# Kernel optimization log

Hardware: AMD Instinct MI355X
Metric: run time of the kernel (lower is better)

Reference implementation:

```python
import jax, jax.numpy as jnp
import numpy as np
from jax import lax

T, B, H = 1024, 128, 512   # num_tokens, batch, encoder hidden
A, K, F = 128, 32, 31      # attention hidden, conv filters, filter length


def setup_inputs() -> dict:
    key = jax.random.key(0)
    ks = jax.random.split(key, 8)
    s = 0.05  # param init scale for numerical stability of tanh
    encoded_tokens = jax.random.normal(ks[0], (T, B, H), jnp.float32)
    query = jax.random.normal(ks[1], (B, H), jnp.float32)
    prev = jax.random.uniform(ks[2], (T, B), jnp.float32)
    previous_alignment = prev / jnp.sum(prev, axis=0, keepdims=True)  # prob-like alignment
    conv_filter = jax.random.normal(ks[3], (K, 1, F), jnp.float32) * s
    W_loc = jax.random.normal(ks[4], (K, A), jnp.float32) * s
    W_q = jax.random.normal(ks[5], (H, A), jnp.float32) * s
    W_k = jax.random.normal(ks[6], (H, A), jnp.float32) * s
    v = jax.random.normal(ks[7], (A,), jnp.float32) * s
    return {"encoded_tokens": encoded_tokens, "query": query,
            "previous_alignment": previous_alignment, "conv_filter": conv_filter,
            "W_loc": W_loc, "W_q": W_q, "W_k": W_k, "v": v}


def reference(encoded_tokens, query, previous_alignment, conv_filter, W_loc, W_q, W_k, v):
    pad = (conv_filter.shape[-1] - 1) // 2
    # Location features: conv1d over token axis of previous alignment.
    # previous_alignment [T,B] -> [B,1,T]; conv_filter [K,1,F] -> loc [B,K,T]
    loc = lax.conv_general_dilated(previous_alignment.T[:, None, :], conv_filter,
                                   window_strides=(1,), padding=[(pad, pad)],
                                   dimension_numbers=("NCH", "OIH", "NCH"))
    proc_loc = jnp.einsum("bkt,ka->tba", loc, W_loc)              # [T,B,A]
    proc_query = query @ W_q                                       # [B,A]
    proc_keys = jnp.einsum("tbh,ha->tba", encoded_tokens, W_k)    # [T,B,A]
    # Additive (Bahdanau) score with tanh nonlinearity.
    score = jnp.einsum("tba,a->tb", jnp.tanh(proc_keys + proc_loc + proc_query[None]), v)
    alignment = jax.nn.softmax(score, axis=0)                      # softmax over tokens [T,B]
    context = jnp.einsum("tb,tbh->bh", alignment, encoded_tokens)  # [B,H]
    return context, alignment
```

## Files before the change

### kernel.cpp

```cpp
#include <hip/hip_runtime.h>
#include <hip/hip_bf16.h>
#include <math.h>

#define T_DIM 1024
#define B_DIM 128
#define H_DIM 512
#define A_DIM 128
#define K_DIM 32
#define F_DIM 31

#define WS_PQ    0
#define WS_SCORE 16384
#define WS_WKHI  147456
#define WS_WKLO  180224
#define WS_WCT   212992
#define WS_PART  147456

typedef __attribute__((ext_vector_type(8)))  short bf16x8;
typedef __attribute__((ext_vector_type(16))) float f32x16;

__device__ __forceinline__ ushort f2bf(float x) {
  unsigned u = __float_as_uint(x);
  u += 0x7FFFu + ((u >> 16) & 1u);
  return (ushort)(u >> 16);
}
__device__ __forceinline__ float bf2f(ushort h) {
  return __uint_as_float(((unsigned)h) << 16);
}
__device__ __forceinline__ float fast_tanh(float x) {
  float xc = fminf(10.f, fmaxf(-10.f, x));
  float e2 = __expf(2.f * xc);
  return __fdividef(e2 - 1.f, e2 + 1.f);
}

__global__ __launch_bounds__(256) void prep_kernel(
    const float* __restrict__ query, const float* __restrict__ conv_filter,
    const float* __restrict__ W_loc, const float* __restrict__ W_q,
    const float* __restrict__ W_k, float* __restrict__ ws)
{
  int blk = blockIdx.x, tid = threadIdx.x;
  if (blk < 128) {
    __shared__ float red[256];
    int a = tid & 127, half = tid >> 7;
    const float* q = query + blk * H_DIM + half * 256;
    const float* w = W_q + (size_t)(half * 256) * A_DIM + a;
    float s = 0.f;
    #pragma unroll 8
    for (int h = 0; h < 256; ++h) s = fmaf(q[h], w[(size_t)h * A_DIM], s);
    red[tid] = s;
    __syncthreads();
    if (tid < 128) ws[WS_PQ + blk * A_DIM + tid] = red[tid] + red[tid + 128];
  } else if (blk == 128) {
    ushort* wct = (ushort*)(ws + WS_WCT);
    for (int it = 0; it < 16; ++it) {
      int e = tid + it * 256;
      int f = e >> 7, a = e & 127;
      float s = 0.f;
      if (f < F_DIM) {
        #pragma unroll
        for (int k = 0; k < K_DIM; ++k)
          s += conv_filter[k * F_DIM + f] * W_loc[k * A_DIM + a];
      }
      wct[a * 32 + f] = f2bf(s);
    }
  } else {
    ushort* wkhi = (ushort*)(ws + WS_WKHI);
    ushort* wklo = (ushort*)(ws + WS_WKLO);
    int h0 = (blk - 129) * 16;
    int a = tid & 127, hh = tid >> 7;
    #pragma unroll
    for (int j = 0; j < 8; ++j) {
      int h = h0 + hh * 8 + j;
      float x = W_k[(size_t)h * A_DIM + a];
      ushort hi = f2bf(x);
      float lo = x - bf2f(hi);
      wkhi[a * H_DIM + h] = hi;
      wklo[a * H_DIM + h] = f2bf(lo);
    }
  }
}

__global__ __launch_bounds__(256, 2) void score_kernel(
    const float* __restrict__ enc, const float* __restrict__ ws_f,
    const float* __restrict__ prev, const float* __restrict__ vvec,
    float* __restrict__ score)
{
  __shared__ ushort smA_hi[256 * 32];
  __shared__ ushort smA_lo[256 * 32];
  __shared__ ushort smB_hi[128 * 32];
  __shared__ ushort smB_lo[128 * 32];
  __shared__ float  prevL[32 * 128];

  const ushort* wkhi = (const ushort*)(ws_f + WS_WKHI);
  const ushort* wklo = (const ushort*)(ws_f + WS_WKLO);
  const ushort* wct  = (const ushort*)(ws_f + WS_WCT);
  const float*  pq   = ws_f + WS_PQ;

  const int tid = threadIdx.x;
  const int t0 = blockIdx.x * 2;
  const int R0 = blockIdx.x * 256;
  const int lane = tid & 63, wv = tid >> 6;
  const int l31 = lane & 31, g = lane >> 5;
  const int wrow = wv * 64;

  f32x16 acc[2][4];
  #pragma unroll
  for (int mf = 0; mf < 2; ++mf)
    #pragma unroll
    for (int nf = 0; nf < 4; ++nf)
      acc[mf][nf] = (f32x16)(0.f);

  #pragma unroll
  for (int it = 0; it < 4; ++it) {
    int seg = tid + it * 256;
    int rr = seg >> 5, c4 = (seg & 31) << 2;
    int t = t0 - 15 + rr;
    float4 val = make_float4(0.f, 0.f, 0.f, 0.f);
    if (t >= 0 && t < T_DIM) val = *(const float4*)(prev + t * B_DIM + c4);
    *(float4*)(prevL + rr * 128 + c4) = val;
  }

  for (int hc = 0; hc < H_DIM; hc += 32) {
    __syncthreads();
    #pragma unroll
    for (int it = 0; it < 8; ++it) {
      int row = it * 32 + (tid >> 3);
      int sub = tid & 7;
      float4 v = *(const float4*)(enc + (size_t)(R0 + row) * H_DIM + hc + sub * 4);
      ushort4 hi4, lo4;
      hi4.x = f2bf(v.x); lo4.x = f2bf(v.x - bf2f(hi4.x));
      hi4.y = f2bf(v.y); lo4.y = f2bf(v.y - bf2f(hi4.y));
      hi4.z = f2bf(v.z); lo4.z = f2bf(v.z - bf2f(hi4.z));
      hi4.w = f2bf(v.w); lo4.w = f2bf(v.w - bf2f(hi4.w));
      int chunk = sub >> 1;
      int boff = row * 64 + ((chunk ^ ((row >> 1) & 3)) << 4) + ((sub & 1) << 3);
      *(ushort4*)((char*)smA_hi + boff) = hi4;
      *(ushort4*)((char*)smA_lo + boff) = lo4;
    }
    #pragma unroll
    for (int it = 0; it < 2; ++it) {
      int a = it * 64 + (tid >> 2);
      int q = tid & 3;
      uint4 vh = *(const uint4*)(wkhi + (size_t)a * H_DIM + hc + q * 8);
      uint4 vl = *(const uint4*)(wklo + (size_t)a * H_DIM + hc + q * 8);
      int boff = a * 64 + ((q ^ ((a >> 1) & 3)) << 4);
      *(uint4*)((char*)smB_hi + boff) = vh;
      *(uint4*)((char*)smB_lo + boff) = vl;
    }
    __syncthreads();
    #pragma unroll
    for (int kk = 0; kk < 2; ++kk) {
      bf16x8 ah[2], al[2];
      #pragma unroll
      for (int mf = 0; mf < 2; ++mf) {
        int row = wrow + mf * 32 + l31;
        int boff = row * 64 + (((kk * 2 + g) ^ ((row >> 1) & 3)) << 4);
        ah[mf] = *(const bf16x8*)((const char*)smA_hi + boff);
        al[mf] = *(const bf16x8*)((const char*)smA_lo + boff);
      }
      #pragma unroll
      for (int nf = 0; nf < 4; ++nf) {
        int a = nf * 32 + l31;
        int boff = a * 64 + (((kk * 2 + g) ^ ((a >> 1) & 3)) << 4);
        bf16x8 bh = *(const bf16x8*)((const char*)smB_hi + boff);
        bf16x8 bl = *(const bf16x8*)((const char*)smB_lo + boff);
        #pragma unroll
        for (int mf = 0; mf < 2; ++mf) {
          acc[mf][nf] = __builtin_amdgcn_mfma_f32_32x32x16_bf16(ah[mf], bh, acc[mf][nf], 0, 0, 0);
          acc[mf][nf] = __builtin_amdgcn_mfma_f32_32x32x16_bf16(ah[mf], bl, acc[mf][nf], 0, 0, 0);
          acc[mf][nf] = __builtin_amdgcn_mfma_f32_32x32x16_bf16(al[mf], bh, acc[mf][nf], 0, 0, 0);
        }
      }
    }
  }

  __syncthreads();
  {
    int trow = tid >> 7, bcol = tid & 127;
    #pragma unroll
    for (int q = 0; q < 4; ++q) {
      bf16x8 pk;
      #pragma unroll
      for (int e = 0; e < 8; ++e) {
        int f = q * 8 + e;
        float pv = (f < F_DIM) ? prevL[(trow + f) * 128 + bcol] : 0.f;
        pk[e] = (short)f2bf(pv);
      }
      int boff = tid * 64 + ((q ^ ((tid >> 1) & 3)) << 4);
      *(bf16x8*)((char*)smA_hi + boff) = pk;
    }
    #pragma unroll
    for (int it = 0; it < 2; ++it) {
      int a = it * 64 + (tid >> 2);
      int q = tid & 3;
      uint4 vv = *(const uint4*)(wct + a * 32 + q * 8);
      *(uint4*)((char*)smB_hi + a * 64 + ((q ^ ((a >> 1) & 3)) << 4)) = vv;
    }
  }
  __syncthreads();
  #pragma unroll
  for (int kk = 0; kk < 2; ++kk) {
    bf16x8 ah[2];
    #pragma unroll
    for (int mf = 0; mf < 2; ++mf) {
      int row = wrow + mf * 32 + l31;
      int boff = row * 64 + (((kk * 2 + g) ^ ((row >> 1) & 3)) << 4);
      ah[mf] = *(const bf16x8*)((const char*)smA_hi + boff);
    }
    #pragma unroll
    for (int nf = 0; nf < 4; ++nf) {
      int a = nf * 32 + l31;
      int boff = a * 64 + (((kk * 2 + g) ^ ((a >> 1) & 3)) << 4);
      bf16x8 bh = *(const bf16x8*)((const char*)smB_hi + boff);
      #pragma unroll
      for (int mf = 0; mf < 2; ++mf)
        acc[mf][nf] = __builtin_amdgcn_mfma_f32_32x32x16_bf16(ah[mf], bh, acc[mf][nf], 0, 0, 0);
    }
  }

  float vval[4];
  #pragma unroll
  for (int nf = 0; nf < 4; ++nf) vval[nf] = vvec[nf * 32 + l31];
  #pragma unroll
  for (int mf = 0; mf < 2; ++mf) {
    #pragma unroll
    for (int reg = 0; reg < 16; ++reg) {
      int row = wrow + mf * 32 + (reg & 3) + 8 * (reg >> 2) + 4 * g;
      int b = row & 127;
      float s = 0.f;
      #pragma unroll
      for (int nf = 0; nf < 4; ++nf) {
        float u = acc[mf][nf][reg] + pq[b * A_DIM + nf * 32 + l31];
        s = fmaf(fast_tanh(u), vval[nf], s);
      }
      s += __shfl_xor(s, 1); s += __shfl_xor(s, 2); s += __shfl_xor(s, 4);
      s += __shfl_xor(s, 8); s += __shfl_xor(s, 16);
      if (l31 == 0) {
        int t = t0 + (row >> 7);
        score[b * T_DIM + t] = s;
      }
    }
  }
}

__global__ __launch_bounds__(256) void softmax_kernel(
    float* __restrict__ score, float* __restrict__ out_align)
{
  __shared__ float red[8];
  int b = blockIdx.x, tid = threadIdx.x;
  float v0[4];
  #pragma unroll
  for (int i = 0; i < 4; ++i) v0[i] = score[b * T_DIM + tid + i * 256];
  float m = fmaxf(fmaxf(v0[0], v0[1]), fmaxf(v0[2], v0[3]));
  #pragma unroll
  for (int off = 1; off < 64; off <<= 1) m = fmaxf(m, __shfl_xor(m, off));
  if ((tid & 63) == 0) red[tid >> 6] = m;
  __syncthreads();
  m = fmaxf(fmaxf(red[0], red[1]), fmaxf(red[2], red[3]));
  float s = 0.f;
  #pragma unroll
  for (int i = 0; i < 4; ++i) { v0[i] = expf(v0[i] - m); s += v0[i]; }
  #pragma unroll
  for (int off = 1; off < 64; off <<= 1) s += __shfl_xor(s, off);
  if ((tid & 63) == 0) red[4 + (tid >> 6)] = s;
  __syncthreads();
  float inv = 1.f / (red[4] + red[5] + red[6] + red[7]);
  #pragma unroll
  for (int i = 0; i < 4; ++i) {
    float a = v0[i] * inv;
    int t = tid + i * 256;
    score[b * T_DIM + t] = a;
    out_align[t * B_DIM + b] = a;
  }
}

__global__ __launch_bounds__(256) void context_partial(
    const float* __restrict__ enc, const float* __restrict__ align_bt,
    float* __restrict__ partial)
{
  int b  = blockIdx.x >> 3;
  int tc = blockIdx.x & 7;
  int tid = threadIdx.x;
  const float* ab = align_bt + b * T_DIM + tc * 128;
  const float* eb = enc + ((size_t)(tc * 128) * B_DIM + b) * H_DIM + tid * 2;
  const size_t stride = (size_t)B_DIM * H_DIM;
  float2 a0 = {0.f, 0.f}, a1 = {0.f, 0.f}, a2 = {0.f, 0.f}, a3 = {0.f, 0.f};
  for (int t = 0; t < 128; t += 4) {
    float4 av = *(const float4*)(ab + t);
    float2 e0 = *(const float2*)(eb + (size_t)(t + 0) * stride);
    float2 e1 = *(const float2*)(eb + (size_t)(t + 1) * stride);
    float2 e2 = *(const float2*)(eb + (size_t)(t + 2) * stride);
    float2 e3 = *(const float2*)(eb + (size_t)(t + 3) * stride);
    a0.x = fmaf(av.x, e0.x, a0.x); a0.y = fmaf(av.x, e0.y, a0.y);
    a1.x = fmaf(av.y, e1.x, a1.x); a1.y = fmaf(av.y, e1.y, a1.y);
    a2.x = fmaf(av.z, e2.x, a2.x); a2.y = fmaf(av.z, e2.y, a2.y);
    a3.x = fmaf(av.w, e3.x, a3.x); a3.y = fmaf(av.w, e3.y, a3.y);
  }
  float2 r;
  r.x = (a0.x + a1.x) + (a2.x + a3.x);
  r.y = (a0.y + a1.y) + (a2.y + a3.y);
  *(float2*)(partial + ((size_t)tc * B_DIM + b) * H_DIM + tid * 2) = r;
}

__global__ __launch_bounds__(256) void context_reduce(
    const float* __restrict__ partial, float* __restrict__ ctx)
{
  int idx = blockIdx.x * 256 + threadIdx.x;
  float s = 0.f;
  #pragma unroll
  for (int tc = 0; tc < 8; ++tc) s += partial[tc * (B_DIM * H_DIM) + idx];
  ctx[idx] = s;
}

extern "C" void kernel_launch(void* const* d_in, const int* in_sizes, int n_in,
                              void* d_out, int out_size, void* d_ws, size_t ws_size,
                              hipStream_t stream)
{
  const float* enc   = (const float*)d_in[0];
  const float* query = (const float*)d_in[1];
  const float* prev  = (const float*)d_in[2];
  const float* filt  = (const float*)d_in[3];
  const float* wloc  = (const float*)d_in[4];
  const float* wq    = (const float*)d_in[5];
  const float* wkp   = (const float*)d_in[6];
  const float* vvec  = (const float*)d_in[7];
  float* out = (float*)d_out;
  float* ws  = (float*)d_ws;

  prep_kernel<<<161, 256, 0, stream>>>(query, filt, wloc, wq, wkp, ws);
  score_kernel<<<512, 256, 0, stream>>>(enc, ws, prev, vvec, ws + WS_SCORE);
  softmax_kernel<<<128, 256, 0, stream>>>(ws + WS_SCORE, out + B_DIM * H_DIM);
  context_partial<<<1024, 256, 0, stream>>>(enc, ws + WS_SCORE, ws + WS_PART);
  context_reduce<<<256, 256, 0, stream>>>(ws + WS_PART, out);
}
```

Measured before the change: 522.9 us.

## Restructure score kernel into small full-K tiles with direct LDS loads

The score kernel now gives each block one token and 32 batch rows with the full 512-wide hidden dimension. That tile is staged into LDS once through global_load_lds with an XOR swizzle, and the bf16 hi/lo split happens in registers just before the MFMA. Each wave owns 32 attention columns and reads W_k directly from global memory, and the four per-wave partial scores are combined through LDS. This removes the per-chunk sync and convert-and-store loop and raises the block count so more blocks are resident. The context partial kernel is also reworked to use float4 loads with 2 batches per block, for better coalescing.

Result: slower. 570.3 us (+9.1%).

```diff
diff --git a/kernel.cpp b/kernel.cpp
--- a/kernel.cpp
+++ b/kernel.cpp
@@ -32,6 +32,10 @@
   float e2 = __expf(2.f * xc);
   return __fdividef(e2 - 1.f, e2 + 1.f);
 }
+
+#define GLOAD16(gsrc, ldsdst) \
+  __builtin_amdgcn_global_load_lds((const __attribute__((address_space(1))) void*)(gsrc), \
+                                   (__attribute__((address_space(3))) void*)(ldsdst), 16, 0, 0)
 
 __global__ __launch_bounds__(256) void prep_kernel(
     const float* __restrict__ query, const float* __restrict__ conv_filter,
@@ -85,11 +89,8 @@
     const float* __restrict__ prev, const float* __restrict__ vvec,
     float* __restrict__ score)
 {
-  __shared__ ushort smA_hi[256 * 32];
-  __shared__ ushort smA_lo[256 * 32];
-  __shared__ ushort smB_hi[128 * 32];
-  __shared__ ushort smB_lo[128 * 32];
-  __shared__ float  prevL[32 * 128];
+  __shared__ float smS[16384];
+  __shared__ float smR[128];
 
   const ushort* wkhi = (const ushort*)(ws_f + WS_WKHI);
   const ushort* wklo = (const ushort*)(ws_f + WS_WKLO);
@@ -97,149 +98,78 @@
   const float*  pq   = ws_f + WS_PQ;
 
   const int tid = threadIdx.x;
-  const int t0 = blockIdx.x * 2;
-  const int R0 = blockIdx.x * 256;
-  const int lane = tid & 63, wv = tid >> 6;
+  const int t0 = blockIdx.x >> 2;
+  const int b0 = (blockIdx.x & 3) << 5;
+  const int lane = tid & 63, w = tid >> 6;
   const int l31 = lane & 31, g = lane >> 5;
-  const int wrow = wv * 64;
-
-  f32x16 acc[2][4];
-  #pragma unroll
-  for (int mf = 0; mf < 2; ++mf)
-    #pragma unroll
-    for (int nf = 0; nf < 4; ++nf)
-      acc[mf][nf] = (f32x16)(0.f);
-
-  #pragma unroll
-  for (int it = 0; it < 4; ++it) {
-    int seg = tid + it * 256;
-    int rr = seg >> 5, c4 = (seg & 31) << 2;
-    int t = t0 - 15 + rr;
-    float4 val = make_float4(0.f, 0.f, 0.f, 0.f);
-    if (t >= 0 && t < T_DIM) val = *(const float4*)(prev + t * B_DIM + c4);
-    *(float4*)(prevL + rr * 128 + c4) = val;
-  }
-
-  for (int hc = 0; hc < H_DIM; hc += 32) {
-    __syncthreads();
-    #pragma unroll
-    for (int it = 0; it < 8; ++it) {
-      int row = it * 32 + (tid >> 3);
-      int sub = tid & 7;
-      float4 v = *(const float4*)(enc + (size_t)(R0 + row) * H_DIM + hc + sub * 4);
-      ushort4 hi4, lo4;
-      hi4.x = f2bf(v.x); lo4.x = f2bf(v.x - bf2f(hi4.x));
-      hi4.y = f2bf(v.y); lo4.y = f2bf(v.y - bf2f(hi4.y));
-      hi4.z = f2bf(v.z); lo4.z = f2bf(v.z - bf2f(hi4.z));
-      hi4.w = f2bf(v.w); lo4.w = f2bf(v.w - bf2f(hi4.w));
-      int chunk = sub >> 1;
-      int boff = row * 64 + ((chunk ^ ((row >> 1) & 3)) << 4) + ((sub & 1) << 3);
-      *(ushort4*)((char*)smA_hi + boff) = hi4;
-      *(ushort4*)((char*)smA_lo + boff) = lo4;
-    }
-    #pragma unroll
-    for (int it = 0; it < 2; ++it) {
-      int a = it * 64 + (tid >> 2);
-      int q = tid & 3;
-      uint4 vh = *(const uint4*)(wkhi + (size_t)a * H_DIM + hc + q * 8);
-      uint4 vl = *(const uint4*)(wklo + (size_t)a * H_DIM + hc + q * 8);
-      int boff = a * 64 + ((q ^ ((a >> 1) & 3)) << 4);
-      *(uint4*)((char*)smB_hi + boff) = vh;
-      *(uint4*)((char*)smB_lo + boff) = vl;
-    }
-    __syncthreads();
-    #pragma unroll
-    for (int kk = 0; kk < 2; ++kk) {
-      bf16x8 ah[2], al[2];
-      #pragma unroll
-      for (int mf = 0; mf < 2; ++mf) {
-        int row = wrow + mf * 32 + l31;
-        int boff = row * 64 + (((kk * 2 + g) ^ ((row >> 1) & 3)) << 4);
-        ah[mf] = *(const bf16x8*)((const char*)smA_hi + boff);
-        al[mf] = *(const bf16x8*)((const char*)smA_lo + boff);
-      }
-      #pragma unroll
-      for (int nf = 0; nf < 4; ++nf) {
-        int a = nf * 32 + l31;
-        int boff = a * 64 + (((kk * 2 + g) ^ ((a >> 1) & 3)) << 4);
-        bf16x8 bh = *(const bf16x8*)((const char*)smB_hi + boff);
-        bf16x8 bl = *(const bf16x8*)((const char*)smB_lo + boff);
-        #pragma unroll
-        for (int mf = 0; mf < 2; ++mf) {
-          acc[mf][nf] = __builtin_amdgcn_mfma_f32_32x32x16_bf16(ah[mf], bh, acc[mf][nf], 0, 0, 0);
-          acc[mf][nf] = __builtin_amdgcn_mfma_f32_32x32x16_bf16(ah[mf], bl, acc[mf][nf], 0, 0, 0);
-          acc[mf][nf] = __builtin_amdgcn_mfma_f32_32x32x16_bf16(al[mf], bh, acc[mf][nf], 0, 0, 0);
-        }
-      }
-    }
-  }
-
-  __syncthreads();
-  {
-    int trow = tid >> 7, bcol = tid & 127;
-    #pragma unroll
-    for (int q = 0; q < 4; ++q) {
-      bf16x8 pk;
-      #pragma unroll
-      for (int e = 0; e < 8; ++e) {
-        int f = q * 8 + e;
-        float pv = (f < F_DIM) ? prevL[(trow + f) * 128 + bcol] : 0.f;
-        pk[e] = (short)f2bf(pv);
-      }
-      int boff = tid * 64 + ((q ^ ((tid >> 1) & 3)) << 4);
-      *(bf16x8*)((char*)smA_hi + boff) = pk;
-    }
-    #pragma unroll
-    for (int it = 0; it < 2; ++it) {
-      int a = it * 64 + (tid >> 2);
-      int q = tid & 3;
-      uint4 vv = *(const uint4*)(wct + a * 32 + q * 8);
-      *(uint4*)((char*)smB_hi + a * 64 + ((q ^ ((a >> 1) & 3)) << 4)) = vv;
-    }
-  }
-  __syncthreads();
-  #pragma unroll
-  for (int kk = 0; kk < 2; ++kk) {
-    bf16x8 ah[2];
-    #pragma unroll
-    for (int mf = 0; mf < 2; ++mf) {
-      int row = wrow + mf * 32 + l31;
-      int boff = row * 64 + (((kk * 2 + g) ^ ((row >> 1) & 3)) << 4);
-      ah[mf] = *(const bf16x8*)((const char*)smA_hi + boff);
-    }
-    #pragma unroll
-    for (int nf = 0; nf < 4; ++nf) {
-      int a = nf * 32 + l31;
-      int boff = a * 64 + (((kk * 2 + g) ^ ((a >> 1) & 3)) << 4);
-      bf16x8 bh = *(const bf16x8*)((const char*)smB_hi + boff);
-      #pragma unroll
-      for (int mf = 0; mf < 2; ++mf)
-        acc[mf][nf] = __builtin_amdgcn_mfma_f32_32x32x16_bf16(ah[mf], bh, acc[mf][nf], 0, 0, 0);
-    }
-  }
-
-  float vval[4];
-  #pragma unroll
-  for (int nf = 0; nf < 4; ++nf) vval[nf] = vvec[nf * 32 + l31];
-  #pragma unroll
-  for (int mf = 0; mf < 2; ++mf) {
-    #pragma unroll
-    for (int reg = 0; reg < 16; ++reg) {
-      int row = wrow + mf * 32 + (reg & 3) + 8 * (reg >> 2) + 4 * g;
-      int b = row & 127;
-      float s = 0.f;
-      #pragma unroll
-      for (int nf = 0; nf < 4; ++nf) {
-        float u = acc[mf][nf][reg] + pq[b * A_DIM + nf * 32 + l31];
-        s = fmaf(fast_tanh(u), vval[nf], s);
-      }
-      s += __shfl_xor(s, 1); s += __shfl_xor(s, 2); s += __shfl_xor(s, 4);
-      s += __shfl_xor(s, 8); s += __shfl_xor(s, 16);
-      if (l31 == 0) {
-        int t = t0 + (row >> 7);
-        score[b * T_DIM + t] = s;
-      }
-    }
+
+  const size_t gbase = ((size_t)t0 * B_DIM + b0) * H_DIM;
+  #pragma unroll
+  for (int i = 0; i < 16; ++i) {
+    int ldsoff = (w << 14) + (i << 10);
+    int d = ldsoff + (lane << 4);
+    int row = d >> 11;
+    int src = (row << 11) + ((d & 2047) ^ (row << 4));
+    GLOAD16(enc + gbase + (src >> 2), &smS[ldsoff >> 2]);
+  }
+  asm volatile("s_waitcnt vmcnt(0)" ::: "memory");
+  __syncthreads();
+
+  const int a_idx = (w << 5) + l31;
+  const ushort* bhp = wkhi + (size_t)a_idx * H_DIM + (g << 3);
+  const ushort* blp = wklo + (size_t)a_idx * H_DIM + (g << 3);
+  const int rswz = l31 << 4;
+  const int rbase = l31 << 11;
+
+  f32x16 acc = (f32x16)(0.f);
+  #pragma unroll 8
+  for (int kk = 0; kk < 32; ++kk) {
+    int a0 = rbase + (((kk << 6) + (g << 5)) ^ rswz);
+    float4 x0 = *(const float4*)((const char*)smS + a0);
+    float4 x1 = *(const float4*)((const char*)smS + (a0 ^ 16));
+    float xs[8] = {x0.x, x0.y, x0.z, x0.w, x1.x, x1.y, x1.z, x1.w};
+    bf16x8 ah, al;
+    #pragma unroll
+    for (int e = 0; e < 8; ++e) {
+      ushort hi = f2bf(xs[e]);
+      ah[e] = (short)hi;
+      al[e] = (short)f2bf(xs[e] - bf2f(hi));
+    }
+    bf16x8 bh = *(const bf16x8*)(bhp + (kk << 4));
+    bf16x8 bl = *(const bf16x8*)(blp + (kk << 4));
+    acc = __builtin_amdgcn_mfma_f32_32x32x16_bf16(ah, bh, acc, 0, 0, 0);
+    acc = __builtin_amdgcn_mfma_f32_32x32x16_bf16(ah, bl, acc, 0, 0, 0);
+    acc = __builtin_amdgcn_mfma_f32_32x32x16_bf16(al, bh, acc, 0, 0, 0);
+  }
+
+  #pragma unroll
+  for (int kt = 0; kt < 2; ++kt) {
+    bf16x8 ap;
+    #pragma unroll
+    for (int e = 0; e < 8; ++e) {
+      int f = (kt << 4) + (g << 3) + e;
+      int t = t0 - 15 + f;
+      float pv = (f < F_DIM && t >= 0 && t < T_DIM) ? prev[t * B_DIM + b0 + l31] : 0.f;
+      ap[e] = (short)f2bf(pv);
+    }
+    bf16x8 bp = *(const bf16x8*)(wct + (a_idx << 5) + (kt << 4) + (g << 3));
+    acc = __builtin_amdgcn_mfma_f32_32x32x16_bf16(ap, bp, acc, 0, 0, 0);
+  }
+
+  float va = vvec[a_idx];
+  #pragma unroll
+  for (int reg = 0; reg < 16; ++reg) {
+    int row = (reg & 3) + ((reg >> 2) << 3) + (g << 2);
+    float u = acc[reg] + pq[(b0 + row) * A_DIM + a_idx];
+    float p = fast_tanh(u) * va;
+    p += __shfl_xor(p, 1); p += __shfl_xor(p, 2); p += __shfl_xor(p, 4);
+    p += __shfl_xor(p, 8); p += __shfl_xor(p, 16);
+    if (l31 == 0) smR[(w << 5) + row] = p;
+  }
+  __syncthreads();
+  if (tid < 32) {
+    float sc = smR[tid] + smR[32 + tid] + smR[64 + tid] + smR[96 + tid];
+    score[(size_t)(b0 + tid) * T_DIM + t0] = sc;
   }
 }
 
@@ -278,28 +208,27 @@
     const float* __restrict__ enc, const float* __restrict__ align_bt,
     float* __restrict__ partial)
 {
-  int b  = blockIdx.x >> 3;
-  int tc = blockIdx.x & 7;
-  int tid = threadIdx.x;
-  const float* ab = align_bt + b * T_DIM + tc * 128;
-  const float* eb = enc + ((size_t)(tc * 128) * B_DIM + b) * H_DIM + tid * 2;
-  const size_t stride = (size_t)B_DIM * H_DIM;
-  float2 a0 = {0.f, 0.f}, a1 = {0.f, 0.f}, a2 = {0.f, 0.f}, a3 = {0.f, 0.f};
-  for (int t = 0; t < 128; t += 4) {
-    float4 av = *(const float4*)(ab + t);
-    float2 e0 = *(const float2*)(eb + (size_t)(t + 0) * stride);
-    float2 e1 = *(const float2*)(eb + (size_t)(t + 1) * stride);
-    float2 e2 = *(const float2*)(eb + (size_t)(t + 2) * stride);
-    float2 e3 = *(const float2*)(eb + (size_t)(t + 3) * stride);
-    a0.x = fmaf(av.x, e0.x, a0.x); a0.y = fmaf(av.x, e0.y, a0.y);
-    a1.x = fmaf(av.y, e1.x, a1.x); a1.y = fmaf(av.y, e1.y, a1.y);
-    a2.x = fmaf(av.z, e2.x, a2.x); a2.y = fmaf(av.z, e2.y, a2.y);
-    a3.x = fmaf(av.w, e3.x, a3.x); a3.y = fmaf(av.w, e3.y, a3.y);
-  }
-  float2 r;
-  r.x = (a0.x + a1.x) + (a2.x + a3.x);
-  r.y = (a0.y + a1.y) + (a2.y + a3.y);
-  *(float2*)(partial + ((size_t)tc * B_DIM + b) * H_DIM + tid * 2) = r;
+  int tq = blockIdx.x >> 6;
+  int bg = blockIdx.x & 63;
+  int bi = threadIdx.x >> 7;
+  int b  = (bg << 1) + bi;
+  int h0 = (threadIdx.x & 127) << 2;
+  const float* ap = align_bt + (size_t)b * T_DIM + (tq << 7);
+  const float* ep = enc + ((size_t)(tq << 7) * B_DIM + b) * H_DIM + h0;
+  const size_t ts = (size_t)B_DIM * H_DIM;
+  float4 acc = make_float4(0.f, 0.f, 0.f, 0.f);
+  for (int t = 0; t < 128; t += 8) {
+    #pragma unroll
+    for (int u2 = 0; u2 < 8; ++u2) {
+      float a = ap[t + u2];
+      float4 e = *(const float4*)(ep + (size_t)(t + u2) * ts);
+      acc.x = fmaf(a, e.x, acc.x);
+      acc.y = fmaf(a, e.y, acc.y);
+      acc.z = fmaf(a, e.z, acc.z);
+      acc.w = fmaf(a, e.w, acc.w);
+    }
+  }
+  *(float4*)(partial + ((size_t)tq * B_DIM + b) * H_DIM + h0) = acc;
 }
 
 __global__ __launch_bounds__(256) void context_reduce(
@@ -328,8 +257,8 @@
   float* ws  = (float*)d_ws;
 
   prep_kernel<<<161, 256, 0, stream>>>(query, filt, wloc, wq, wkp, ws);
-  score_kernel<<<512, 256, 0, stream>>>(enc, ws, prev, vvec, ws + WS_SCORE);
+  score_kernel<<<4096, 256, 0, stream>>>(enc, ws, prev, vvec, ws + WS_SCORE);
   softmax_kernel<<<128, 256, 0, stream>>>(ws + WS_SCORE, out + B_DIM * H_DIM);
-  context_partial<<<1024, 256, 0, stream>>>(enc, ws + WS_SCORE, ws + WS_PART);
+  context_partial<<<512, 256, 0, stream>>>(enc, ws + WS_SCORE, ws + WS_PART);
   context_reduce<<<256, 256, 0, stream>>>(ws + WS_PART, out);
 }
```
